# Performance work log

Measured on AMD Instinct MI355X. Metric: run time of the kernel, lower is better.

Reference implementation:

```python
import jax, jax.numpy as jnp
import numpy as np
from jax import lax

B, S, D, K, H, NSLOT = 16, 128, 64, 64, 128, 96  # batch, seq/context, input, inter, hidden, slots


def setup_inputs() -> dict:
    key = jax.random.key(0)
    k = jax.random.split(key, 7)
    x_contexts = jax.random.normal(k[0], (B, S, D), jnp.float32)
    time_contexts = jax.random.randint(k[1], (B, S, S), 0, NSLOT + 1)
    dist_contexts = jax.random.randint(k[2], (B, S, S), 0, NSLOT + 1)
    context_masks = jax.random.randint(k[3], (B, S, S), 0, 2).astype(bool)
    # xavier-normal style init, matching nn.init.xavier_normal_ scales
    time_weights = jax.random.normal(k[4], (NSLOT + 1, D, K), jnp.float32) * (2.0 / (D + K)) ** 0.5
    dist_weights = jax.random.normal(k[5], (NSLOT + 1, K, H), jnp.float32) * (2.0 / (K + H)) ** 0.5
    hidden_weights = jax.random.normal(k[6], (H, H), jnp.float32) * (2.0 / (H + H)) ** 0.5
    return {"x_contexts": x_contexts, "time_contexts": time_contexts,
            "dist_contexts": dist_contexts, "context_masks": context_masks,
            "time_weights": time_weights, "dist_weights": dist_weights,
            "hidden_weights": hidden_weights}


def reference(x_contexts, time_contexts, dist_contexts, context_masks,
              time_weights, dist_weights, hidden_weights):
    # x_contexts: (B,S,D); *_contexts: (B,S,S) int; context_masks: (B,S,S) bool
    Bb, Ss, Dd = x_contexts.shape
    Hh = hidden_weights.shape[0]
    pos = jnp.arange(Ss)

    def step(h, xs):
        t_idx, d_idx, m, i = xs  # t_idx,d_idx,m: (B,S); i: step index
        # original slices context to :i+1; equivalent jit-friendly form: mask out j>i
        valid = m & (pos[None, :] <= i)  # (B,S)
        Tw = time_weights[t_idx]  # (B,S,D,K) gather
        Dw = dist_weights[d_idx]  # (B,S,K,H) gather
        # x @ (Tw @ Dw) reassociated as (x @ Tw) @ Dw to avoid (B,S,D,H) intermediate
        xt = jnp.einsum('bsd,bsdk->bsk', x_contexts, Tw)
        xc = jnp.einsum('bsk,bskh->bsh', xt, Dw)
        xc = jnp.where(valid[..., None], xc, 0.0).sum(axis=1)  # (B,H)
        h_new = jax.nn.sigmoid(xc + h @ hidden_weights)
        return h_new, h_new

    h0 = jnp.zeros((Bb, Hh), x_contexts.dtype)
    xs = (jnp.swapaxes(time_contexts, 0, 1),
          jnp.swapaxes(dist_contexts, 0, 1),
          jnp.swapaxes(context_masks, 0, 1),
          jnp.arange(Ss))
    hT, outs = lax.scan(step, h0, xs)
    # outputs: (B,S,H), final hidden with leading unsqueezed dim: (1,B,H)
    return jnp.swapaxes(outs, 0, 1), hT[None]
```

## Files before the change

kernel.cpp:

```cpp
#include <hip/hip_runtime.h>
#include <math.h>


#define B_ 16
#define S_ 128
#define D_ 64
#define K_ 64
#define H_ 128
#define NS 97
#define NB 64
#define MAXE 132096

#define XC_OFF 0
#define BH_T   262144
#define BH_D   (BH_T + NS * NB)
#define CNT_T  (BH_D + NS * NB)
#define CNT_D  (CNT_T + NS)
#define CNT_B  (CNT_D + NS)
#define OFF_T  (CNT_B + 2048)
#define OFF_D  (OFF_T + 98)
#define OFF_B  (OFF_D + 98)
#define ENT_T  291464
#define ENT_DX (ENT_T + MAXE)
#define ENT_DP (ENT_DX + MAXE)
#define XT16_OFF (ENT_DP + MAXE)
#define Y16_OFF  (XT16_OFF + MAXE * 32)
#define NEED_BYTES ((size_t)(Y16_OFF + (size_t)MAXE * 64) * 4)

typedef _Float16 h2_t __attribute__((ext_vector_type(2)));
typedef _Float16 f16x8 __attribute__((ext_vector_type(8)));
typedef float f32x4 __attribute__((ext_vector_type(4)));

#if __has_builtin(__builtin_amdgcn_fdot2)
#define FDOT2(a, b, c) __builtin_amdgcn_fdot2((a), (b), (c), false)
#else
#define FDOT2(a, b, c) ((c) + (float)(a)[0] * (float)(b)[0] + (float)(a)[1] * (float)(b)[1])
#endif


__global__ __launch_bounds__(256) void k_hist1(const int* __restrict__ tc,
                                               const int* __restrict__ dc,
                                               const int* __restrict__ mk,
                                               unsigned* wsi) {
    __shared__ unsigned ht[NS], hd[NS], hb[32];
    int tid = threadIdx.x, blk = blockIdx.x;
    if (tid < NS) { ht[tid] = 0; hd[tid] = 0; }
    if (tid < 32) hb[tid] = 0;
    __syncthreads();
    int base = blk * 4096;
    #pragma unroll
    for (int u = 0; u < 16; u++) {
        int idx = base + tid + u * 256;
        int i = (idx >> 7) & 127, j = idx & 127;
        if (j <= i && mk[idx] != 0) {
            atomicAdd(&ht[tc[idx]], 1u);
            atomicAdd(&hd[dc[idx]], 1u);
            atomicAdd(&hb[(idx >> 7) & 31], 1u);
        }
    }
    __syncthreads();
    if (tid < NS) {
        wsi[BH_T + tid * NB + blk] = ht[tid];
        wsi[BH_D + tid * NB + blk] = hd[tid];
    }
    if (tid < 32) wsi[CNT_B + blk * 32 + tid] = hb[tid];
}

template <int CH>
__device__ unsigned scan_region(unsigned* in, unsigned* out, int L, unsigned* s) {
    int tid = threadIdx.x;
    unsigned loc[CH], sum = 0;
    #pragma unroll
    for (int k = 0; k < CH; k++) {
        int idx = tid * CH + k;
        loc[k] = (idx < L) ? in[idx] : 0u;
        sum += loc[k];
    }
    s[tid] = sum;
    __syncthreads();
    for (int o = 1; o < 1024; o <<= 1) {
        unsigned a = (tid >= o) ? s[tid - o] : 0u;
        __syncthreads();
        s[tid] += a;
        __syncthreads();
    }
    unsigned total = s[1023];
    unsigned run = s[tid] - sum;
    __syncthreads();
    #pragma unroll
    for (int k = 0; k < CH; k++) {
        int idx = tid * CH + k;
        if (idx < L) { out[idx] = run; run += loc[k]; }
    }
    __syncthreads();
    return total;
}

__global__ __launch_bounds__(1024) void k_scan_all(unsigned* wsi) {
    __shared__ unsigned s[1024];
    int tid = threadIdx.x;

    unsigned tot = scan_region<13>(wsi + BH_T, wsi + BH_T, 2 * NS * NB, s);
    unsigned totT = wsi[BH_D];
    if (tid < NS) {
        unsigned b0 = wsi[BH_T + tid * NB];
        unsigned b1 = (tid < NS - 1) ? wsi[BH_T + (tid + 1) * NB] : totT;
        wsi[OFF_T + tid] = b0;
        wsi[CNT_T + tid] = b1 - b0;
        unsigned d0 = wsi[BH_D + tid * NB];
        unsigned d1 = (tid < NS - 1) ? wsi[BH_D + (tid + 1) * NB] : tot;
        wsi[OFF_D + tid] = d0 - totT;
        wsi[CNT_D + tid] = d1 - d0;
    }
    if (tid == 0) { wsi[OFF_T + NS] = totT; wsi[OFF_D + NS] = tot - totT; }
    __syncthreads();

    unsigned totB = scan_region<2>(wsi + CNT_B, wsi + OFF_B, 2048, s);
    if (tid == 0) wsi[OFF_B + 2048] = totB;
}

__global__ __launch_bounds__(256) void k_scatter(const int* __restrict__ tc,
                                                 const int* __restrict__ dc,
                                                 const int* __restrict__ mk,
                                                 unsigned* wsi, int useY) {
    __shared__ unsigned ct[NS], cd[NS], cb[32];
    int tid = threadIdx.x, blk = blockIdx.x;
    unsigned totT = wsi[OFF_T + NS];
    if (tid < NS) {
        ct[tid] = wsi[BH_T + tid * NB + blk];
        cd[tid] = wsi[BH_D + tid * NB + blk] - totT;
    }
    if (tid < 32) cb[tid] = wsi[OFF_B + blk * 32 + tid];
    __syncthreads();
    int base = blk * 4096;
    #pragma unroll
    for (int u = 0; u < 16; u++) {
        int idx = base + tid + u * 256;
        int i = (idx >> 7) & 127, j = idx & 127, b = idx >> 14;
        if (j <= i && mk[idx] != 0) {
            unsigned t = (unsigned)tc[idx], d = (unsigned)dc[idx];
            unsigned tpos = atomicAdd(&ct[t], 1u);
            wsi[ENT_T + tpos] = (unsigned)b | ((unsigned)i << 4) | ((unsigned)j << 11)
                              | (t << 18) | (d << 25);
            unsigned dpos = atomicAdd(&cd[d], 1u);
            unsigned yp = useY ? atomicAdd(&cb[(idx >> 7) & 31], 1u) : (unsigned)(idx >> 7);
            wsi[ENT_DX + dpos] = tpos;
            wsi[ENT_DP + dpos] = yp;
        }
    }
}

__global__ __launch_bounds__(256) void k_phaseA(const float* __restrict__ x,
                                                const float* __restrict__ tw,
                                                unsigned* wsi, float* wsf) {
    int t = blockIdx.x, c = blockIdx.y;
    int rows = (int)wsi[CNT_T + t] - c * 128;
    if (rows <= 0) return;
    if (rows > 128) rows = 128;
    unsigned base = wsi[OFF_T + t] + c * 128;

    __shared__ float stw[4096];
    __shared__ float sx[8192];
    __shared__ unsigned ent[128];
    int tid = threadIdx.x;

    const float4* twg = (const float4*)(tw + t * 4096);
    float4* stw4 = (float4*)stw;
    #pragma unroll
    for (int q = 0; q < 4; q++) stw4[q * 256 + tid] = twg[q * 256 + tid];
    if (tid < 128) ent[tid] = (tid < rows) ? wsi[ENT_T + base + tid] : 0u;
    __syncthreads();

    int lane16 = tid & 15, rquot = tid >> 4;
    #pragma unroll
    for (int p = 0; p < 8; p++) {
        int r = p * 16 + rquot;
        float4 v = make_float4(0.f, 0.f, 0.f, 0.f);
        if (r < rows) {
            unsigned e = ent[r];
            int b = e & 15, j = (e >> 11) & 127;
            v = *(const float4*)(x + (b * S_ + j) * D_ + lane16 * 4);
        }
        int col4 = lane16 ^ (r & 15);
        float* dst = &sx[r * 64 + col4 * 4];
        dst[0] = v.x; dst[1] = v.y; dst[2] = v.z; dst[3] = v.w;
    }
    __syncthreads();

    int rgrp = tid & 15, cgrp = tid >> 4;
    float4 acc[8];
    #pragma unroll
    for (int i = 0; i < 8; i++) acc[i] = make_float4(0.f, 0.f, 0.f, 0.f);
    #pragma unroll 4
    for (int dd = 0; dd < 64; dd++) {
        float4 w = stw4[dd * 16 + cgrp];
        int s_idx = (((dd >> 2) ^ rgrp) << 2) + (dd & 3);
        #pragma unroll
        for (int i = 0; i < 8; i++) {
            float a = sx[(rgrp + 16 * i) * 64 + s_idx];
            acc[i].x += a * w.x; acc[i].y += a * w.y;
            acc[i].z += a * w.z; acc[i].w += a * w.w;
        }
    }
    _Float16* XT = (_Float16*)(wsf + XT16_OFF);
    #pragma unroll
    for (int i = 0; i < 8; i++) {
        int r = rgrp + 16 * i;
        if (r < rows) {
            union { _Float16 h[4]; double d64; } u;
            u.h[0] = (_Float16)acc[i].x; u.h[1] = (_Float16)acc[i].y;
            u.h[2] = (_Float16)acc[i].z; u.h[3] = (_Float16)acc[i].w;
            *(double*)&XT[(size_t)(base + r) * 64 + cgrp * 4] = u.d64;
        }
    }
}

__global__ __launch_bounds__(256) void k_phaseB(const float* __restrict__ dw,
                                                unsigned* wsi, float* wsf, int useY) {
    int d = blockIdx.x, c = blockIdx.y;
    int rows = (int)wsi[CNT_D + d] - c * 128;
    if (rows <= 0) return;
    if (rows > 128) rows = 128;
    unsigned base = wsi[OFF_D + d] + c * 128;

    __shared__ _Float16 sa[128 * 64];
    __shared__ _Float16 sb[64 * 128];
    __shared__ unsigned entx_s[128], entp_s[128];
    int tid = threadIdx.x;

    if (tid < 128) {
        entx_s[tid] = (tid < rows) ? wsi[ENT_DX + base + tid] : 0u;
        entp_s[tid] = (tid < rows) ? wsi[ENT_DP + base + tid] : 0u;
    }
    const float4* dwg = (const float4*)(dw + (size_t)d * 8192);
    #pragma unroll
    for (int q = 0; q < 8; q++) {
        float4 v = dwg[q * 256 + tid];
        union { _Float16 h[4]; double d64; } u;
        u.h[0] = (_Float16)v.x; u.h[1] = (_Float16)v.y;
        u.h[2] = (_Float16)v.z; u.h[3] = (_Float16)v.w;
        *(double*)&sb[(q * 256 + tid) * 4] = u.d64;
    }
    __syncthreads();

    {
        int r = tid >> 1, hh = tid & 1;
        const _Float16* XT = (const _Float16*)(wsf + XT16_OFF);
        const f16x8* src = (const f16x8*)(XT + (size_t)entx_s[r] * 64 + hh * 32);
        #pragma unroll
        for (int mm = 0; mm < 4; mm++) {
            f16x8 hv = {0, 0, 0, 0, 0, 0, 0, 0};
            if (r < rows) hv = src[mm];
            int chunk = hh * 4 + mm;
            *(f16x8*)&sa[r * 64 + (chunk ^ (r & 7)) * 8] = hv;
        }
    }
    __syncthreads();

    int w = tid >> 6, lane = tid & 63;
    int l15 = lane & 15, lg = lane >> 4;
    f16x8 bf[2][2];
    #pragma unroll
    for (int n = 0; n < 2; n++) {
        int col = w * 32 + n * 16 + l15;
        #pragma unroll
        for (int ks = 0; ks < 2; ks++) {
            int kb = ks * 32 + lg * 8;
            f16x8 t;
            #pragma unroll
            for (int e = 0; e < 8; e++) t[e] = sb[(kb + e) * 128 + col];
            bf[n][ks] = t;
        }
    }
    f32x4 acc[8][2];
    f32x4 z = {0.f, 0.f, 0.f, 0.f};
    #pragma unroll
    for (int m = 0; m < 8; m++) { acc[m][0] = z; acc[m][1] = z; }

    #pragma unroll
    for (int m = 0; m < 8; m++) {
        int row = m * 16 + l15;
        f16x8 a0 = *(f16x8*)&sa[row * 64 + ((lg) ^ (row & 7)) * 8];
        f16x8 a1 = *(f16x8*)&sa[row * 64 + ((4 + lg) ^ (row & 7)) * 8];
        #pragma unroll
        for (int n = 0; n < 2; n++) {
            acc[m][n] = __builtin_amdgcn_mfma_f32_16x16x32_f16(a0, bf[n][0], acc[m][n], 0, 0, 0);
            acc[m][n] = __builtin_amdgcn_mfma_f32_16x16x32_f16(a1, bf[n][1], acc[m][n], 0, 0, 0);
        }
    }

    if (useY) {
        _Float16* Y16 = (_Float16*)(wsf + Y16_OFF);
        #pragma unroll
        for (int m = 0; m < 8; m++) {
            #pragma unroll
            for (int reg = 0; reg < 4; reg++) {
                int row = m * 16 + lg * 4 + reg;
                if (row < rows) {
                    _Float16* p = Y16 + (size_t)entp_s[row] * 128 + w * 32 + l15;
                    p[0]  = (_Float16)acc[m][0][reg];
                    p[16] = (_Float16)acc[m][1][reg];
                }
            }
        }
    } else {
        float* XC = wsf + XC_OFF;
        #pragma unroll
        for (int m = 0; m < 8; m++) {
            #pragma unroll
            for (int reg = 0; reg < 4; reg++) {
                int row = m * 16 + lg * 4 + reg;
                if (row < rows) {
                    float* p = XC + (size_t)entp_s[row] * 128 + w * 32 + l15;
                    atomicAdd(p + 0,  acc[m][0][reg]);
                    atomicAdd(p + 16, acc[m][1][reg]);
                }
            }
        }
    }
}

__global__ __launch_bounds__(128) void k_reduce(unsigned* wsi, float* wsf) {
    __shared__ float part[8][128];
    int bi = blockIdx.x, tid = threadIdx.x;
    unsigned n = wsi[CNT_B + bi], off = wsi[OFF_B + bi];
    int rq = tid >> 4, cs = tid & 15;
    const _Float16* Yb = (const _Float16*)(wsf + Y16_OFF) + (size_t)off * 128 + cs * 8;
    float a0 = 0.f, a1 = 0.f, a2 = 0.f, a3 = 0.f;
    float a4 = 0.f, a5 = 0.f, a6 = 0.f, a7 = 0.f;
    for (unsigned e = rq; e < n; e += 8) {
        f16x8 v = *(const f16x8*)&Yb[(size_t)e * 128];
        a0 += (float)v[0]; a1 += (float)v[1]; a2 += (float)v[2]; a3 += (float)v[3];
        a4 += (float)v[4]; a5 += (float)v[5]; a6 += (float)v[6]; a7 += (float)v[7];
    }
    float* pp = &part[rq][cs * 8];
    pp[0] = a0; pp[1] = a1; pp[2] = a2; pp[3] = a3;
    pp[4] = a4; pp[5] = a5; pp[6] = a6; pp[7] = a7;
    __syncthreads();
    float s = (part[0][tid] + part[1][tid]) + (part[2][tid] + part[3][tid])
            + (part[4][tid] + part[5][tid]) + (part[6][tid] + part[7][tid]);
    wsf[XC_OFF + (size_t)bi * 128 + tid] = s;
}

#define RSTEP(XCREG, IDX, CURB)                                                \
    {                                                                          \
        float xc_use = XCREG;                                                  \
        if (kh == 0 && i + 4 + (IDX) < 128) XCREG = XC[(i + 4 + (IDX)) * 128]; \
        const float4* hb = (const float4*)&h16[CURB][kh * 32];                 \
        float a0 = 0.f, a1 = 0.f, a2 = 0.f, a3 = 0.f;                          \
        _Pragma("unroll")                                                      \
        for (int q = 0; q < 8; q++) {                                          \
            union { float4 f4; h2_t h2[4]; } u;                                \
            u.f4 = hb[q];                                                      \
            a0 = FDOT2(u.h2[0], w2[4 * q + 0], a0);                            \
            a1 = FDOT2(u.h2[1], w2[4 * q + 1], a1);                            \
            a2 = FDOT2(u.h2[2], w2[4 * q + 2], a2);                            \
            a3 = FDOT2(u.h2[3], w2[4 * q + 3], a3);                            \
        }                                                                      \
        float p = (a0 + a1) + (a2 + a3);                                       \
        p += __shfl_xor(p, 32);                                                \
        if (kh == 0) {                                                         \
            float v = xc_use + p;                                              \
            v = 1.f / (1.f + __expf(-v));                                      \
            val = v;                                                           \
            ((_Float16*)&h16[(CURB) ^ 1][0])[col] = (_Float16)v;               \
            out[(size_t)(b * 128 + i + (IDX)) * 128 + col] = v;                \
        }                                                                      \
        __syncthreads();                                                       \
    }

__global__ __launch_bounds__(256) void k_recur(const float* __restrict__ hw,
                                               const float* __restrict__ wsf,
                                               float* __restrict__ out) {
    int b = blockIdx.x;
    __shared__ h2_t h16[2][64];
    int tid = threadIdx.x;
    int lane = tid & 63, wv = tid >> 6;
    int c32 = lane & 31, kh = lane >> 5;
    int col = wv * 32 + c32;
    int k0 = kh * 64;

    h2_t w2[32];
    #pragma unroll
    for (int m = 0; m < 32; m++) {
        h2_t p;
        p[0] = (_Float16)hw[(k0 + 2 * m) * 128 + col];
        p[1] = (_Float16)hw[(k0 + 2 * m + 1) * 128 + col];
        w2[m] = p;
    }
    if (tid < 64) h16[0][tid] = (h2_t)(_Float16)0.f;
    __syncthreads();

    const float* XC = wsf + XC_OFF + (size_t)b * 128 * 128 + col;
    float xc0 = 0.f, xc1 = 0.f, xc2 = 0.f, xc3 = 0.f;
    if (kh == 0) {
        xc0 = XC[0 * 128]; xc1 = XC[1 * 128];
        xc2 = XC[2 * 128]; xc3 = XC[3 * 128];
    }
    float val = 0.f;
    for (int i = 0; i < 128; i += 4) {
        RSTEP(xc0, 0, 0)
        RSTEP(xc1, 1, 1)
        RSTEP(xc2, 2, 0)
        RSTEP(xc3, 3, 1)
    }
    if (kh == 0) out[(size_t)B_ * S_ * H_ + b * 128 + col] = val;
}

extern "C" void kernel_launch(void* const* d_in, const int* in_sizes, int n_in,
                              void* d_out, int out_size, void* d_ws, size_t ws_size,
                              hipStream_t stream) {
    const float* x  = (const float*)d_in[0];
    const int*   tc = (const int*)d_in[1];
    const int*   dc = (const int*)d_in[2];
    const int*   mk = (const int*)d_in[3];
    const float* tw = (const float*)d_in[4];
    const float* dw = (const float*)d_in[5];
    const float* hw = (const float*)d_in[6];
    float*    out = (float*)d_out;
    float*    wsf = (float*)d_ws;
    unsigned* wsi = (unsigned*)d_ws;
    char*     wsb = (char*)d_ws;

    int useY = (ws_size >= NEED_BYTES) ? 1 : 0;
    if (!useY)
        hipMemsetAsync(wsb, 0, (size_t)262144 * 4, stream);

    k_hist1<<<dim3(NB), dim3(256), 0, stream>>>(tc, dc, mk, wsi);
    k_scan_all<<<dim3(1), dim3(1024), 0, stream>>>(wsi);
    k_scatter<<<dim3(NB), dim3(256), 0, stream>>>(tc, dc, mk, wsi, useY);
    k_phaseA<<<dim3(NS, 16), dim3(256), 0, stream>>>(x, tw, wsi, wsf);
    k_phaseB<<<dim3(NS, 16), dim3(256), 0, stream>>>(dw, wsi, wsf, useY);
    if (useY) k_reduce<<<dim3(2048), dim3(128), 0, stream>>>(wsi, wsf);
    k_recur<<<dim3(16), dim3(256), 0, stream>>>(hw, wsf, out);
}
```

Measured before the change: 137.6 us.

## Fuse histogram, scan and scatter into one cooperative kernel with grid sync

```diff
diff --git a/kernel.cpp b/kernel.cpp
--- a/kernel.cpp
+++ b/kernel.cpp
@@ -1,5 +1,8 @@
 #include <hip/hip_runtime.h>
+#include <hip/hip_cooperative_groups.h>
 #include <math.h>
+
+namespace cg = cooperative_groups;
 
 
 #define B_ 16
@@ -37,37 +40,8 @@
 #define FDOT2(a, b, c) ((c) + (float)(a)[0] * (float)(b)[0] + (float)(a)[1] * (float)(b)[1])
 #endif
 
-
-__global__ __launch_bounds__(256) void k_hist1(const int* __restrict__ tc,
-                                               const int* __restrict__ dc,
-                                               const int* __restrict__ mk,
-                                               unsigned* wsi) {
-    __shared__ unsigned ht[NS], hd[NS], hb[32];
-    int tid = threadIdx.x, blk = blockIdx.x;
-    if (tid < NS) { ht[tid] = 0; hd[tid] = 0; }
-    if (tid < 32) hb[tid] = 0;
-    __syncthreads();
-    int base = blk * 4096;
-    #pragma unroll
-    for (int u = 0; u < 16; u++) {
-        int idx = base + tid + u * 256;
-        int i = (idx >> 7) & 127, j = idx & 127;
-        if (j <= i && mk[idx] != 0) {
-            atomicAdd(&ht[tc[idx]], 1u);
-            atomicAdd(&hd[dc[idx]], 1u);
-            atomicAdd(&hb[(idx >> 7) & 31], 1u);
-        }
-    }
-    __syncthreads();
-    if (tid < NS) {
-        wsi[BH_T + tid * NB + blk] = ht[tid];
-        wsi[BH_D + tid * NB + blk] = hd[tid];
-    }
-    if (tid < 32) wsi[CNT_B + blk * 32 + tid] = hb[tid];
-}
-
 template <int CH>
-__device__ unsigned scan_region(unsigned* in, unsigned* out, int L, unsigned* s) {
+__device__ unsigned scan256(unsigned* in, unsigned* out, int L, unsigned* s) {
     int tid = threadIdx.x;
     unsigned loc[CH], sum = 0;
     #pragma unroll
@@ -78,13 +52,13 @@
     }
     s[tid] = sum;
     __syncthreads();
-    for (int o = 1; o < 1024; o <<= 1) {
+    for (int o = 1; o < 256; o <<= 1) {
         unsigned a = (tid >= o) ? s[tid - o] : 0u;
         __syncthreads();
         s[tid] += a;
         __syncthreads();
     }
-    unsigned total = s[1023];
+    unsigned total = s[255];
     unsigned run = s[tid] - sum;
     __syncthreads();
     #pragma unroll
@@ -96,35 +70,66 @@
     return total;
 }
 
-__global__ __launch_bounds__(1024) void k_scan_all(unsigned* wsi) {
-    __shared__ unsigned s[1024];
-    int tid = threadIdx.x;
-
-    unsigned tot = scan_region<13>(wsi + BH_T, wsi + BH_T, 2 * NS * NB, s);
-    unsigned totT = wsi[BH_D];
+__global__ __launch_bounds__(256) void k_bin(const int* __restrict__ tc,
+                                             const int* __restrict__ dc,
+                                             const int* __restrict__ mk,
+                                             unsigned* wsi, int useY) {
+    __shared__ unsigned ht[NS], hd[NS], hb[32];
+    __shared__ unsigned char t8[4096], d8[4096];
+    __shared__ unsigned s[256];
+    int tid = threadIdx.x, blk = blockIdx.x;
+    cg::grid_group grid = cg::this_grid();
+
+    if (tid < NS) { ht[tid] = 0; hd[tid] = 0; }
+    if (tid < 32) hb[tid] = 0;
+    __syncthreads();
+    int base = blk * 4096;
+    #pragma unroll 4
+    for (int u = 0; u < 16; u++) {
+        int li = tid + u * 256;
+        int idx = base + li;
+        int i = (idx >> 7) & 127, j = idx & 127;
+        unsigned char tv = 0xFF, dv = 0;
+        if (j <= i && mk[idx] != 0) {
+            tv = (unsigned char)tc[idx];
+            dv = (unsigned char)dc[idx];
+            atomicAdd(&ht[tv], 1u);
+            atomicAdd(&hd[dv], 1u);
+            atomicAdd(&hb[(idx >> 7) & 31], 1u);
+        }
+        t8[li] = tv; d8[li] = dv;
+    }
+    __syncthreads();
     if (tid < NS) {
-        unsigned b0 = wsi[BH_T + tid * NB];
-        unsigned b1 = (tid < NS - 1) ? wsi[BH_T + (tid + 1) * NB] : totT;
-        wsi[OFF_T + tid] = b0;
-        wsi[CNT_T + tid] = b1 - b0;
-        unsigned d0 = wsi[BH_D + tid * NB];
-        unsigned d1 = (tid < NS - 1) ? wsi[BH_D + (tid + 1) * NB] : tot;
-        wsi[OFF_D + tid] = d0 - totT;
-        wsi[CNT_D + tid] = d1 - d0;
-    }
-    if (tid == 0) { wsi[OFF_T + NS] = totT; wsi[OFF_D + NS] = tot - totT; }
-    __syncthreads();
-
-    unsigned totB = scan_region<2>(wsi + CNT_B, wsi + OFF_B, 2048, s);
-    if (tid == 0) wsi[OFF_B + 2048] = totB;
-}
-
-__global__ __launch_bounds__(256) void k_scatter(const int* __restrict__ tc,
-                                                 const int* __restrict__ dc,
-                                                 const int* __restrict__ mk,
-                                                 unsigned* wsi, int useY) {
+        wsi[BH_T + tid * NB + blk] = ht[tid];
+        wsi[BH_D + tid * NB + blk] = hd[tid];
+    }
+    if (tid < 32) wsi[CNT_B + blk * 32 + tid] = hb[tid];
+
+    grid.sync();
+
+    if (blk == 0) {
+        unsigned tot = scan256<49>(wsi + BH_T, wsi + BH_T, 2 * NS * NB, s);
+        unsigned totT = wsi[BH_D];
+        if (tid < NS) {
+            unsigned b0 = wsi[BH_T + tid * NB];
+            unsigned b1 = (tid < NS - 1) ? wsi[BH_T + (tid + 1) * NB] : totT;
+            wsi[OFF_T + tid] = b0;
+            wsi[CNT_T + tid] = b1 - b0;
+            unsigned d0 = wsi[BH_D + tid * NB];
+            unsigned d1 = (tid < NS - 1) ? wsi[BH_D + (tid + 1) * NB] : tot;
+            wsi[OFF_D + tid] = d0 - totT;
+            wsi[CNT_D + tid] = d1 - d0;
+        }
+        if (tid == 0) { wsi[OFF_T + NS] = totT; wsi[OFF_D + NS] = tot - totT; }
+        __syncthreads();
+        unsigned totB = scan256<8>(wsi + CNT_B, wsi + OFF_B, 2048, s);
+        if (tid == 0) wsi[OFF_B + 2048] = totB;
+    }
+
+    grid.sync();
+
     __shared__ unsigned ct[NS], cd[NS], cb[32];
-    int tid = threadIdx.x, blk = blockIdx.x;
     unsigned totT = wsi[OFF_T + NS];
     if (tid < NS) {
         ct[tid] = wsi[BH_T + tid * NB + blk];
@@ -132,13 +137,14 @@
     }
     if (tid < 32) cb[tid] = wsi[OFF_B + blk * 32 + tid];
     __syncthreads();
-    int base = blk * 4096;
-    #pragma unroll
+    #pragma unroll 4
     for (int u = 0; u < 16; u++) {
-        int idx = base + tid + u * 256;
-        int i = (idx >> 7) & 127, j = idx & 127, b = idx >> 14;
-        if (j <= i && mk[idx] != 0) {
-            unsigned t = (unsigned)tc[idx], d = (unsigned)dc[idx];
+        int li = tid + u * 256;
+        int idx = base + li;
+        unsigned char tv = t8[li];
+        if (tv != 0xFF) {
+            unsigned t = tv, d = d8[li];
+            int i = (idx >> 7) & 127, j = idx & 127, b = idx >> 14;
             unsigned tpos = atomicAdd(&ct[t], 1u);
             wsi[ENT_T + tpos] = (unsigned)b | ((unsigned)i << 4) | ((unsigned)j << 11)
                               | (t << 18) | (d << 25);
@@ -410,10 +416,10 @@
 extern "C" void kernel_launch(void* const* d_in, const int* in_sizes, int n_in,
                               void* d_out, int out_size, void* d_ws, size_t ws_size,
                               hipStream_t stream) {
-    const float* x  = (const float*)d_in[0];
     const int*   tc = (const int*)d_in[1];
     const int*   dc = (const int*)d_in[2];
     const int*   mk = (const int*)d_in[3];
+    const float* x  = (const float*)d_in[0];
     const float* tw = (const float*)d_in[4];
     const float* dw = (const float*)d_in[5];
     const float* hw = (const float*)d_in[6];
@@ -426,9 +432,10 @@
     if (!useY)
         hipMemsetAsync(wsb, 0, (size_t)262144 * 4, stream);
 
-    k_hist1<<<dim3(NB), dim3(256), 0, stream>>>(tc, dc, mk, wsi);
-    k_scan_all<<<dim3(1), dim3(1024), 0, stream>>>(wsi);
-    k_scatter<<<dim3(NB), dim3(256), 0, stream>>>(tc, dc, mk, wsi, useY);
+    {
+        void* args[] = { (void*)&tc, (void*)&dc, (void*)&mk, (void*)&wsi, (void*)&useY };
+        hipLaunchCooperativeKernel((void*)k_bin, dim3(NB), dim3(256), args, 0, stream);
+    }
     k_phaseA<<<dim3(NS, 16), dim3(256), 0, stream>>>(x, tw, wsi, wsf);
     k_phaseB<<<dim3(NS, 16), dim3(256), 0, stream>>>(dw, wsi, wsf, useY);
     if (useY) k_reduce<<<dim3(2048), dim3(128), 0, stream>>>(wsi, wsf);
```

New measurement: 155.5 us. 13.0% more time.
